# Optimization experiments

Hardware: AMD Instinct MI355X
Metric: run time of the kernel (lower is better)

Reference implementation:

```python
import jax, jax.numpy as jnp
import numpy as np

NUM_HEADS = 8


def setup_inputs() -> dict:
    key = jax.random.key(0)
    ks = jax.random.split(key, 8)
    B, N, D, H = 4, 1200, 256, NUM_HEADS
    return {
        "query_bbox": jax.random.normal(ks[0], (B, N, 10), jnp.float32) * 20.0,
        "query_feat": jax.random.normal(ks[1], (B, N, D), jnp.float32),
        "beta_w": jax.random.normal(ks[2], (H, D), jnp.float32) * 0.02,
        "beta_b": jax.random.uniform(ks[3], (H,), jnp.float32, 0.0, 2.0),
        "in_proj_w": jax.random.normal(ks[4], (3 * D, D), jnp.float32) * (D ** -0.5),
        "in_proj_b": jnp.zeros((3 * D,), jnp.float32),
        "out_proj_w": jax.random.normal(ks[5], (D, D), jnp.float32) * (D ** -0.5),
        "out_proj_b": jnp.zeros((D,), jnp.float32),
    }


def reference(query_bbox, query_feat, beta_w, beta_b, in_proj_w, in_proj_b,
              out_proj_w, out_proj_b):
    B, N, D = query_feat.shape
    H = NUM_HEADS
    hd = D // H

    # center_dists (no_grad in original): negative pairwise L2 of bbox centers
    centers = jax.lax.stop_gradient(query_bbox[..., :2])            # [B,N,2]
    diff = centers[:, :, None, :] - centers[:, None, :, :]          # [B,N,N,2]
    dist = -jnp.sqrt(jnp.sum(diff * diff, axis=-1))                 # [B,N,N]

    # per-head learned beta scale
    beta = jnp.einsum('bnd,hd->bhn', query_feat, beta_w) + beta_b[None, :, None]  # [B,H,N]
    attn_mask = dist[:, None, :, :] * beta[..., None]               # [B,H,N,N]

    # multi-head self-attention with additive mask
    qkv = jnp.einsum('bnd,ed->bne', query_feat, in_proj_w) + in_proj_b
    q, k, v = jnp.split(qkv, 3, axis=-1)
    q = q.reshape(B, N, H, hd)
    k = k.reshape(B, N, H, hd)
    v = v.reshape(B, N, H, hd)

    scores = jnp.einsum('bqhd,bkhd->bhqk', q, k) * (hd ** -0.5) + attn_mask
    attn = jax.nn.softmax(scores, axis=-1)                          # [B,H,N,N]
    out = jnp.einsum('bhqk,bkhd->bqhd', attn, v).reshape(B, N, D)
    return jnp.einsum('bnd,ed->bne', out, out_proj_w) + out_proj_b
```

## Files before the change

### kernel.cpp

```cpp
#include <hip/hip_runtime.h>
#include <hip/hip_bf16.h>

#define BC 4
#define NQ 1200
#define DIM 256
#define NH 8
#define HD 32
#define E3 768
#define MROWS (BC*NQ)
#define SCALE 0.17677669529663687f
#define L2E 1.4426950408889634f

typedef __attribute__((ext_vector_type(8))) short bf16x8;
typedef __attribute__((ext_vector_type(4))) float f32x4;

__device__ inline short f2bf(float f) {
    __hip_bfloat16 h = __float2bfloat16(f);
    return *reinterpret_cast<short*>(&h);
}
__device__ inline unsigned pack2bf(float a, float b) {
    unsigned ua = (unsigned short)f2bf(a);
    unsigned ub = (unsigned short)f2bf(b);
    return ua | (ub << 16);
}

__global__ void beta_ctr_kernel(const float* __restrict__ feat, const float* __restrict__ bw,
                                const float* __restrict__ bb, const float* __restrict__ bbox,
                                float* __restrict__ beta, float* __restrict__ ctr) {
    int gw = (blockIdx.x * 256 + threadIdx.x) >> 6;
    int lane = threadIdx.x & 63;
    if (gw >= MROWS) return;
    const float* frow = feat + (size_t)gw * DIM;
    float acc[NH];
#pragma unroll
    for (int h = 0; h < NH; ++h) acc[h] = 0.f;
#pragma unroll
    for (int it = 0; it < DIM / 64; ++it) {
        int d = it * 64 + lane;
        float f = frow[d];
#pragma unroll
        for (int h = 0; h < NH; ++h) acc[h] += f * bw[h * DIM + d];
    }
#pragma unroll
    for (int h = 0; h < NH; ++h) {
#pragma unroll
        for (int off = 32; off; off >>= 1) acc[h] += __shfl_xor(acc[h], off);
    }
    int b = gw / NQ, n = gw % NQ;
#pragma unroll
    for (int h = 0; h < NH; ++h) {
        float v = acc[h] + bb[h];
        if (lane == h) beta[(b * NH + h) * NQ + n] = v;
    }
    if (lane == 0) {
        ctr[gw * 2]     = bbox[(size_t)gw * 10];
        ctr[gw * 2 + 1] = bbox[(size_t)gw * 10 + 1];
    }
}

template<bool AF32, bool BF32, bool OUTF32>
__global__ __launch_bounds__(256) void gemm_k256(const void* __restrict__ Av,
                                                 const void* __restrict__ Bv,
                                                 const float* __restrict__ bias,
                                                 void* __restrict__ Cout, int Edim) {
    __shared__ short as[64][40];
    __shared__ short bs[64][40];
    int m0 = blockIdx.y * 64, e0 = blockIdx.x * 64;
    int t = threadIdx.x, lane = t & 63, wid = t >> 6;
    int wr = (wid >> 1) * 32, wc = (wid & 1) * 32;
    f32x4 acc[2][2] = {};
    int lrow = t >> 2, lch = t & 3;

    for (int ks = 0; ks < DIM / 32; ++ks) {
        bf16x8 av, wv;
        if (AF32) {
            const float* A = (const float*)Av;
            float4 f0 = *(const float4*)(A + (size_t)(m0 + lrow) * DIM + ks * 32 + lch * 8);
            float4 f1 = *(const float4*)(A + (size_t)(m0 + lrow) * DIM + ks * 32 + lch * 8 + 4);
            av[0]=f2bf(f0.x); av[1]=f2bf(f0.y); av[2]=f2bf(f0.z); av[3]=f2bf(f0.w);
            av[4]=f2bf(f1.x); av[5]=f2bf(f1.y); av[6]=f2bf(f1.z); av[7]=f2bf(f1.w);
        } else {
            av = *(const bf16x8*)((const short*)Av + (size_t)(m0 + lrow) * DIM + ks * 32 + lch * 8);
        }
        if (BF32) {
            const float* B = (const float*)Bv;
            float4 f0 = *(const float4*)(B + (size_t)(e0 + lrow) * DIM + ks * 32 + lch * 8);
            float4 f1 = *(const float4*)(B + (size_t)(e0 + lrow) * DIM + ks * 32 + lch * 8 + 4);
            wv[0]=f2bf(f0.x); wv[1]=f2bf(f0.y); wv[2]=f2bf(f0.z); wv[3]=f2bf(f0.w);
            wv[4]=f2bf(f1.x); wv[5]=f2bf(f1.y); wv[6]=f2bf(f1.z); wv[7]=f2bf(f1.w);
        } else {
            wv = *(const bf16x8*)((const short*)Bv + (size_t)(e0 + lrow) * DIM + ks * 32 + lch * 8);
        }
        __syncthreads();
        *(bf16x8*)&as[lrow][lch * 8] = av;
        *(bf16x8*)&bs[lrow][lch * 8] = wv;
        __syncthreads();
#pragma unroll
        for (int sm = 0; sm < 2; ++sm) {
            bf16x8 af = *(const bf16x8*)&as[wr + sm * 16 + (lane & 15)][(lane >> 4) * 8];
#pragma unroll
            for (int sn = 0; sn < 2; ++sn) {
                bf16x8 bfv = *(const bf16x8*)&bs[wc + sn * 16 + (lane & 15)][(lane >> 4) * 8];
                acc[sm][sn] = __builtin_amdgcn_mfma_f32_16x16x32_bf16(af, bfv, acc[sm][sn], 0, 0, 0);
            }
        }
    }
#pragma unroll
    for (int sm = 0; sm < 2; ++sm)
#pragma unroll
        for (int sn = 0; sn < 2; ++sn) {
            int e = e0 + wc + sn * 16 + (lane & 15);
            float bv = bias[e];
#pragma unroll
            for (int r = 0; r < 4; ++r) {
                int m = m0 + wr + sm * 16 + (lane >> 4) * 4 + r;
                float v = acc[sm][sn][r] + bv;
                if (OUTF32) ((float*)Cout)[(size_t)m * Edim + e] = v;
                else        ((short*)Cout)[(size_t)m * Edim + e] = f2bf(v);
            }
        }
}

__global__ __launch_bounds__(256) void attn_kernel(const short* __restrict__ qkv,
                                                   const float* __restrict__ beta,
                                                   const float* __restrict__ ctr,
                                                   short* __restrict__ attnb) {
    __shared__ short kt[128][40];
    __shared__ short vt[32][136];
    __shared__ float2 ckv[128];
    __shared__ short pl[4][16][72];

    const int t = threadIdx.x, lane = t & 63, w = t >> 6;
    const int g = lane >> 4, i = lane & 15;
    const int qg = w >> 1, ksp = w & 1;
    const int bh = blockIdx.y, b = bh >> 3, h = bh & 7;
    const int q0 = blockIdx.x * 32 + qg * 16;
    const int q = q0 + i, qc = min(q, NQ - 1);
    const int kwb = ksp * 64;

    bf16x8 qf = *(const bf16x8*)(qkv + (size_t)(b * NQ + qc) * E3 + h * HD + g * 8);
    const float cqx = ctr[(b * NQ + qc) * 2];
    const float cqy = ctr[(b * NQ + qc) * 2 + 1];
    const float bql = beta[(b * NH + h) * NQ + qc] * L2E;
    const float SL2E = SCALE * L2E;

    float mcur = -1e30f, lsum = 0.f;
    f32x4 o0 = {}, o1 = {};
    f32x4 zero = {};

    const int skey = t >> 1, shalf = t & 1;
    const short* kbase = qkv + (size_t)b * NQ * E3 + DIM + h * HD + shalf * 16;
    const short* vbase = qkv + (size_t)b * NQ * E3 + 2 * DIM + h * HD + shalf * 16;

    for (int kb = 0; kb < NQ; kb += 128) {
        __syncthreads();
        {
            int kn = min(kb + skey, NQ - 1);
            bf16x8 kv0 = *(const bf16x8*)(kbase + (size_t)kn * E3);
            bf16x8 kv1 = *(const bf16x8*)(kbase + (size_t)kn * E3 + 8);
            bf16x8 vv0 = *(const bf16x8*)(vbase + (size_t)kn * E3);
            bf16x8 vv1 = *(const bf16x8*)(vbase + (size_t)kn * E3 + 8);
            *(bf16x8*)&kt[skey][shalf * 16]     = kv0;
            *(bf16x8*)&kt[skey][shalf * 16 + 8] = kv1;
#pragma unroll
            for (int j = 0; j < 8; ++j) vt[shalf * 16 + j][skey]     = vv0[j];
#pragma unroll
            for (int j = 0; j < 8; ++j) vt[shalf * 16 + 8 + j][skey] = vv1[j];
            if (t < 128) {
                int c = min(kb + t, NQ - 1);
                ckv[t] = make_float2(ctr[(b * NQ + c) * 2], ctr[(b * NQ + c) * 2 + 1]);
            }
        }
        __syncthreads();

        float st[16];
#pragma unroll
        for (int kc = 0; kc < 4; ++kc) {
            bf16x8 af = *(const bf16x8*)&kt[kwb + kc * 16 + i][g * 8];
            f32x4 s = __builtin_amdgcn_mfma_f32_16x16x32_bf16(af, qf, zero, 0, 0, 0);
            float4 c01 = *(const float4*)&ckv[kwb + kc * 16 + 4 * g];
            float4 c23 = *(const float4*)&ckv[kwb + kc * 16 + 4 * g + 2];
            int kg0 = kb + kwb + kc * 16 + 4 * g;
            float cx[4] = {c01.x, c01.z, c23.x, c23.z};
            float cy[4] = {c01.y, c01.w, c23.y, c23.w};
#pragma unroll
            for (int r = 0; r < 4; ++r) {
                float dx = cqx - cx[r], dy = cqy - cy[r];
                float dist = __builtin_amdgcn_sqrtf(dx * dx + dy * dy);
                float sc = s[r] * SL2E - dist * bql;
                st[kc * 4 + r] = (kg0 + r < NQ) ? sc : -1e30f;
            }
        }
        float vm = st[0];
#pragma unroll
        for (int x = 1; x < 16; ++x) vm = fmaxf(vm, st[x]);
        vm = fmaxf(vm, __shfl_xor(vm, 16));
        vm = fmaxf(vm, __shfl_xor(vm, 32));
        float mnew = fmaxf(mcur, vm);
        float alpha = __builtin_amdgcn_exp2f(mcur - mnew);
        mcur = mnew;
        float rs = 0.f;
#pragma unroll
        for (int x = 0; x < 16; ++x) {
            st[x] = __builtin_amdgcn_exp2f(st[x] - mnew);
            rs += st[x];
        }
        rs += __shfl_xor(rs, 16);
        rs += __shfl_xor(rs, 32);
        lsum = lsum * alpha + rs;
#pragma unroll
        for (int r = 0; r < 4; ++r) { o0[r] *= alpha; o1[r] *= alpha; }
#pragma unroll
        for (int kc = 0; kc < 4; ++kc) {
            *(unsigned*)&pl[w][i][kc * 16 + 4 * g]     = pack2bf(st[kc * 4 + 0], st[kc * 4 + 1]);
            *(unsigned*)&pl[w][i][kc * 16 + 4 * g + 2] = pack2bf(st[kc * 4 + 2], st[kc * 4 + 3]);
        }
#pragma unroll
        for (int kc2 = 0; kc2 < 2; ++kc2) {
            bf16x8 pf  = *(const bf16x8*)&pl[w][i][kc2 * 32 + g * 8];
            bf16x8 vf0 = *(const bf16x8*)&vt[i][kwb + kc2 * 32 + g * 8];
            bf16x8 vf1 = *(const bf16x8*)&vt[16 + i][kwb + kc2 * 32 + g * 8];
            o0 = __builtin_amdgcn_mfma_f32_16x16x32_bf16(vf0, pf, o0, 0, 0, 0);
            o1 = __builtin_amdgcn_mfma_f32_16x16x32_bf16(vf1, pf, o1, 0, 0, 0);
        }
    }

    __syncthreads();
    float* mrg = (float*)&kt[0][0];
    float* my = mrg + (w * 64 + lane) * 10;
    my[0] = mcur; my[1] = lsum;
#pragma unroll
    for (int r = 0; r < 4; ++r) { my[2 + r] = o0[r]; my[6 + r] = o1[r]; }
    __syncthreads();
    const float* pr = mrg + ((w ^ 1) * 64 + lane) * 10;
    float m2 = pr[0], l2 = pr[1];
    float mN = fmaxf(mcur, m2);
    float a1 = __builtin_amdgcn_exp2f(mcur - mN);
    float a2 = __builtin_amdgcn_exp2f(m2 - mN);
    float inv = 1.f / (lsum * a1 + l2 * a2);
    int hh = w & 1;
    f32x4 mine = hh ? o1 : o0;
    if (q < NQ) {
        short4 outv;
        float vals[4];
#pragma unroll
        for (int r = 0; r < 4; ++r) vals[r] = (mine[r] * a1 + pr[2 + hh * 4 + r] * a2) * inv;
        outv.x = f2bf(vals[0]); outv.y = f2bf(vals[1]);
        outv.z = f2bf(vals[2]); outv.w = f2bf(vals[3]);
        *(short4*)&attnb[(size_t)(b * NQ + q) * DIM + h * HD + hh * 16 + 4 * g] = outv;
    }
}

extern "C" void kernel_launch(void* const* d_in, const int* in_sizes, int n_in,
                              void* d_out, int out_size, void* d_ws, size_t ws_size,
                              hipStream_t stream) {
    const float* bbox  = (const float*)d_in[0];
    const float* feat  = (const float*)d_in[1];
    const float* bw    = (const float*)d_in[2];
    const float* bb    = (const float*)d_in[3];
    const float* in_w  = (const float*)d_in[4];
    const float* in_b  = (const float*)d_in[5];
    const float* out_w = (const float*)d_in[6];
    const float* out_b = (const float*)d_in[7];
    float* out = (float*)d_out;

    char* ws = (char*)d_ws;
    size_t off = 0;
    auto alloc = [&](size_t bytes) { void* p = ws + off; off += (bytes + 255) & ~255ull; return p; };
    short* qkvb  = (short*)alloc((size_t)MROWS * E3 * 2);
    short* attnb = (short*)alloc((size_t)MROWS * DIM * 2);
    float* betab = (float*)alloc((size_t)BC * NH * NQ * 4);
    float* ctr   = (float*)alloc((size_t)BC * NQ * 2 * 4);
    (void)ws_size; (void)in_sizes; (void)n_in; (void)out_size;

    beta_ctr_kernel<<<MROWS / 4, 256, 0, stream>>>(feat, bw, bb, bbox, betab, ctr);
    gemm_k256<true, true, false><<<dim3(E3 / 64, MROWS / 64), 256, 0, stream>>>(feat, in_w, in_b, qkvb, E3);
    attn_kernel<<<dim3((NQ + 31) / 32, BC * NH), 256, 0, stream>>>(qkvb, betab, ctr, attnb);
    gemm_k256<false, true, true><<<dim3(DIM / 64, MROWS / 64), 256, 0, stream>>>(attnb, out_w, out_b, out, DIM);
}
```

Before: 68.20 us.

## Emit transposed V from QKV GEMM and read K/V directly from global in attention

```diff
diff --git a/kernel.cpp b/kernel.cpp
--- a/kernel.cpp
+++ b/kernel.cpp
@@ -8,6 +8,7 @@
 #define HD 32
 #define E3 768
 #define MROWS (BC*NQ)
+#define KPAD 1280
 #define SCALE 0.17677669529663687f
 #define L2E 1.4426950408889634f
 
@@ -58,11 +59,12 @@
     }
 }
 
-template<bool AF32, bool BF32, bool OUTF32>
+template<bool AF32, bool BF32, bool OUTF32, bool VTOUT>
 __global__ __launch_bounds__(256) void gemm_k256(const void* __restrict__ Av,
                                                  const void* __restrict__ Bv,
                                                  const float* __restrict__ bias,
-                                                 void* __restrict__ Cout, int Edim) {
+                                                 void* __restrict__ Cout, int Edim,
+                                                 short* __restrict__ vtout) {
     __shared__ short as[64][40];
     __shared__ short bs[64][40];
     int m0 = blockIdx.y * 64, e0 = blockIdx.x * 64;
@@ -111,24 +113,35 @@
         for (int sn = 0; sn < 2; ++sn) {
             int e = e0 + wc + sn * 16 + (lane & 15);
             float bv = bias[e];
-#pragma unroll
-            for (int r = 0; r < 4; ++r) {
-                int m = m0 + wr + sm * 16 + (lane >> 4) * 4 + r;
-                float v = acc[sm][sn][r] + bv;
-                if (OUTF32) ((float*)Cout)[(size_t)m * Edim + e] = v;
-                else        ((short*)Cout)[(size_t)m * Edim + e] = f2bf(v);
+            float vals[4];
+            int mbase = m0 + wr + sm * 16 + (lane >> 4) * 4;
+#pragma unroll
+            for (int r = 0; r < 4; ++r) vals[r] = acc[sm][sn][r] + bv;
+            if (VTOUT && e >= 2 * DIM) {
+                int dv = e - 2 * DIM;
+                int hv = dv >> 5, dd = dv & 31;
+                int bb = mbase / NQ, nn = mbase - bb * NQ;
+                short4 o;
+                o.x = f2bf(vals[0]); o.y = f2bf(vals[1]);
+                o.z = f2bf(vals[2]); o.w = f2bf(vals[3]);
+                *(short4*)&vtout[(((size_t)bb * NH + hv) * HD + dd) * KPAD + nn] = o;
+            } else {
+#pragma unroll
+                for (int r = 0; r < 4; ++r) {
+                    int m = mbase + r;
+                    if (OUTF32) ((float*)Cout)[(size_t)m * Edim + e] = vals[r];
+                    else        ((short*)Cout)[(size_t)m * Edim + e] = f2bf(vals[r]);
+                }
             }
         }
 }
 
 __global__ __launch_bounds__(256) void attn_kernel(const short* __restrict__ qkv,
+                                                   const short* __restrict__ vt,
                                                    const float* __restrict__ beta,
                                                    const float* __restrict__ ctr,
                                                    short* __restrict__ attnb) {
-    __shared__ short kt[128][40];
-    __shared__ short vt[32][136];
-    __shared__ float2 ckv[128];
-    __shared__ short pl[4][16][72];
+    __shared__ __align__(16) char smem[10240];
 
     const int t = threadIdx.x, lane = t & 63, w = t >> 6;
     const int g = lane >> 4, i = lane & 15;
@@ -146,51 +159,34 @@
 
     float mcur = -1e30f, lsum = 0.f;
     f32x4 o0 = {}, o1 = {};
-    f32x4 zero = {};
-
-    const int skey = t >> 1, shalf = t & 1;
-    const short* kbase = qkv + (size_t)b * NQ * E3 + DIM + h * HD + shalf * 16;
-    const short* vbase = qkv + (size_t)b * NQ * E3 + 2 * DIM + h * HD + shalf * 16;
+
+    const short* kgb = qkv + (size_t)b * NQ * E3 + DIM + h * HD + g * 8;
+    const short* vrow = vt + (((size_t)b * NH + h) * HD + i) * KPAD + kwb + g * 8;
+    const float* cgb = ctr + (size_t)b * NQ * 2;
+    short* plw = (short*)smem + w * (16 * 72);
 
     for (int kb = 0; kb < NQ; kb += 128) {
-        __syncthreads();
-        {
-            int kn = min(kb + skey, NQ - 1);
-            bf16x8 kv0 = *(const bf16x8*)(kbase + (size_t)kn * E3);
-            bf16x8 kv1 = *(const bf16x8*)(kbase + (size_t)kn * E3 + 8);
-            bf16x8 vv0 = *(const bf16x8*)(vbase + (size_t)kn * E3);
-            bf16x8 vv1 = *(const bf16x8*)(vbase + (size_t)kn * E3 + 8);
-            *(bf16x8*)&kt[skey][shalf * 16]     = kv0;
-            *(bf16x8*)&kt[skey][shalf * 16 + 8] = kv1;
-#pragma unroll
-            for (int j = 0; j < 8; ++j) vt[shalf * 16 + j][skey]     = vv0[j];
-#pragma unroll
-            for (int j = 0; j < 8; ++j) vt[shalf * 16 + 8 + j][skey] = vv1[j];
-            if (t < 128) {
-                int c = min(kb + t, NQ - 1);
-                ckv[t] = make_float2(ctr[(b * NQ + c) * 2], ctr[(b * NQ + c) * 2 + 1]);
-            }
-        }
-        __syncthreads();
-
         float st[16];
 #pragma unroll
         for (int kc = 0; kc < 4; ++kc) {
-            bf16x8 af = *(const bf16x8*)&kt[kwb + kc * 16 + i][g * 8];
+            int kr = min(kb + kwb + kc * 16 + i, NQ - 1);
+            bf16x8 af = *(const bf16x8*)(kgb + (size_t)kr * E3);
+            f32x4 zero = {};
             f32x4 s = __builtin_amdgcn_mfma_f32_16x16x32_bf16(af, qf, zero, 0, 0, 0);
-            float4 c01 = *(const float4*)&ckv[kwb + kc * 16 + 4 * g];
-            float4 c23 = *(const float4*)&ckv[kwb + kc * 16 + 4 * g + 2];
-            int kg0 = kb + kwb + kc * 16 + 4 * g;
-            float cx[4] = {c01.x, c01.z, c23.x, c23.z};
-            float cy[4] = {c01.y, c01.w, c23.y, c23.w};
+            int kidx = kb + kwb + kc * 16 + 4 * g;
+            float4 cA = *(const float4*)(cgb + kidx * 2);
+            float4 cB = *(const float4*)(cgb + kidx * 2 + 4);
+            float cxv[4] = {cA.x, cA.z, cB.x, cB.z};
+            float cyv[4] = {cA.y, cA.w, cB.y, cB.w};
 #pragma unroll
             for (int r = 0; r < 4; ++r) {
-                float dx = cqx - cx[r], dy = cqy - cy[r];
+                float dx = cqx - cxv[r], dy = cqy - cyv[r];
                 float dist = __builtin_amdgcn_sqrtf(dx * dx + dy * dy);
                 float sc = s[r] * SL2E - dist * bql;
-                st[kc * 4 + r] = (kg0 + r < NQ) ? sc : -1e30f;
+                st[kc * 4 + r] = (kidx + r < NQ) ? sc : -1e30f;
             }
         }
+
         float vm = st[0];
 #pragma unroll
         for (int x = 1; x < 16; ++x) vm = fmaxf(vm, st[x]);
@@ -210,23 +206,30 @@
         lsum = lsum * alpha + rs;
 #pragma unroll
         for (int r = 0; r < 4; ++r) { o0[r] *= alpha; o1[r] *= alpha; }
+
 #pragma unroll
         for (int kc = 0; kc < 4; ++kc) {
-            *(unsigned*)&pl[w][i][kc * 16 + 4 * g]     = pack2bf(st[kc * 4 + 0], st[kc * 4 + 1]);
-            *(unsigned*)&pl[w][i][kc * 16 + 4 * g + 2] = pack2bf(st[kc * 4 + 2], st[kc * 4 + 3]);
-        }
-#pragma unroll
-        for (int kc2 = 0; kc2 < 2; ++kc2) {
-            bf16x8 pf  = *(const bf16x8*)&pl[w][i][kc2 * 32 + g * 8];
-            bf16x8 vf0 = *(const bf16x8*)&vt[i][kwb + kc2 * 32 + g * 8];
-            bf16x8 vf1 = *(const bf16x8*)&vt[16 + i][kwb + kc2 * 32 + g * 8];
-            o0 = __builtin_amdgcn_mfma_f32_16x16x32_bf16(vf0, pf, o0, 0, 0, 0);
-            o1 = __builtin_amdgcn_mfma_f32_16x16x32_bf16(vf1, pf, o1, 0, 0, 0);
-        }
+            *(unsigned*)&plw[i * 72 + kc * 16 + 4 * g]     = pack2bf(st[kc * 4 + 0], st[kc * 4 + 1]);
+            *(unsigned*)&plw[i * 72 + kc * 16 + 4 * g + 2] = pack2bf(st[kc * 4 + 2], st[kc * 4 + 3]);
+        }
+
+        const short* vp = vrow + kb;
+        bf16x8 vf00 = *(const bf16x8*)(vp);
+        bf16x8 vf01 = *(const bf16x8*)(vp + 32);
+        bf16x8 vf10 = *(const bf16x8*)(vp + 16 * KPAD);
+        bf16x8 vf11 = *(const bf16x8*)(vp + 16 * KPAD + 32);
+
+        bf16x8 pbf0 = *(const bf16x8*)&plw[i * 72 + 0 * 32 + g * 8];
+        bf16x8 pbf1 = *(const bf16x8*)&plw[i * 72 + 1 * 32 + g * 8];
+
+        o0 = __builtin_amdgcn_mfma_f32_16x16x32_bf16(vf00, pbf0, o0, 0, 0, 0);
+        o1 = __builtin_amdgcn_mfma_f32_16x16x32_bf16(vf10, pbf0, o1, 0, 0, 0);
+        o0 = __builtin_amdgcn_mfma_f32_16x16x32_bf16(vf01, pbf1, o0, 0, 0, 0);
+        o1 = __builtin_amdgcn_mfma_f32_16x16x32_bf16(vf11, pbf1, o1, 0, 0, 0);
     }
 
     __syncthreads();
-    float* mrg = (float*)&kt[0][0];
+    float* mrg = (float*)smem;
     float* my = mrg + (w * 64 + lane) * 10;
     my[0] = mcur; my[1] = lsum;
 #pragma unroll
@@ -268,13 +271,14 @@
     size_t off = 0;
     auto alloc = [&](size_t bytes) { void* p = ws + off; off += (bytes + 255) & ~255ull; return p; };
     short* qkvb  = (short*)alloc((size_t)MROWS * E3 * 2);
+    short* vtb   = (short*)alloc((size_t)BC * NH * HD * KPAD * 2);
     short* attnb = (short*)alloc((size_t)MROWS * DIM * 2);
     float* betab = (float*)alloc((size_t)BC * NH * NQ * 4);
-    float* ctr   = (float*)alloc((size_t)BC * NQ * 2 * 4);
+    float* ctr   = (float*)alloc((size_t)BC * NQ * 2 * 4 + 1024);
     (void)ws_size; (void)in_sizes; (void)n_in; (void)out_size;
 
     beta_ctr_kernel<<<MROWS / 4, 256, 0, stream>>>(feat, bw, bb, bbox, betab, ctr);
-    gemm_k256<true, true, false><<<dim3(E3 / 64, MROWS / 64), 256, 0, stream>>>(feat, in_w, in_b, qkvb, E3);
-    attn_kernel<<<dim3((NQ + 31) / 32, BC * NH), 256, 0, stream>>>(qkvb, betab, ctr, attnb);
-    gemm_k256<false, true, true><<<dim3(DIM / 64, MROWS / 64), 256, 0, stream>>>(attnb, out_w, out_b, out, DIM);
-}
+    gemm_k256<true, true, false, true><<<dim3(E3 / 64, MROWS / 64), 256, 0, stream>>>(feat, in_w, in_b, qkvb, E3, vtb);
+    attn_kernel<<<dim3((NQ + 31) / 32, BC * NH), 256, 0, stream>>>(qkvb, vtb, betab, ctr, attnb);
+    gemm_k256<false, true, true, false><<<dim3(DIM / 64, MROWS / 64), 256, 0, stream>>>(attnb, out_w, out_b, out, DIM, nullptr);
+}
```

Result: slower. 91.36 us (+34.0%).
